# Kernel tuning notes

Hardware: AMD Instinct MI355X
Metric: run time of the kernel (lower is better)

## Reference

```python
import jax, jax.numpy as jnp
import numpy as np

B, S, N_EMBD = 4, 4096, 1024
HIDDEN = 4 * N_EMBD
M_BITS_FC = 3
M_BITS_PROJ = 3
BLOCK_K = 32


def block_quant(v, m_bits, bk):
    """Block-floating-point quantization along the last (K) dim.
    Each block of `bk` elements shares an exponent derived from its max-abs;
    mantissas are rounded to `m_bits` bits. Straight-through estimator for grads."""
    *lead, K = v.shape
    vb = v.reshape(*lead, K // bk, bk)
    amax = jnp.max(jnp.abs(vb), axis=-1, keepdims=True)
    tiny = jnp.asarray(2.0 ** -126, v.dtype)
    e = jnp.floor(jnp.log2(jnp.maximum(amax, tiny)))  # shared block exponent
    scale = jnp.exp2(e - m_bits)                       # quantization step
    q = jnp.round(vb / scale) * scale
    q = vb + jax.lax.stop_gradient(q - vb)             # STE
    return q.reshape(v.shape)


def lowprec_linear(x, w, b, m_bits, bk):
    # w: [out, in]; quantize both operands along the contraction dim.
    xq = block_quant(x, m_bits, bk)
    wq = block_quant(w, m_bits, bk)
    return jnp.einsum('bsk,nk->bsn', xq, wq) + b


def setup_inputs() -> dict:
    key = jax.random.key(0)
    k0, k1, k2 = jax.random.split(key, 3)
    x = jax.random.normal(k0, (B, S, N_EMBD), jnp.float32)
    w_fc = jax.random.normal(k1, (HIDDEN, N_EMBD), jnp.float32) * (1.0 / np.sqrt(N_EMBD))
    b_fc = jnp.zeros((HIDDEN,), jnp.float32)
    w_proj = jax.random.normal(k2, (N_EMBD, HIDDEN), jnp.float32) * (1.0 / np.sqrt(HIDDEN))
    b_proj = jnp.zeros((N_EMBD,), jnp.float32)
    return {"x": x, "w_fc": w_fc, "b_fc": b_fc, "w_proj": w_proj, "b_proj": b_proj}


def reference(x, w_fc, b_fc, w_proj, b_proj):
    h = lowprec_linear(x, w_fc, b_fc, M_BITS_FC, BLOCK_K)
    h = jax.nn.gelu(h, approximate=False)  # nn.GELU default = exact erf
    return lowprec_linear(h, w_proj, b_proj, M_BITS_PROJ, BLOCK_K)
```

## Files before the change

### kernel.cpp

```cpp
#include <hip/hip_runtime.h>
#include <hip/hip_bf16.h>

using bf16 = __hip_bfloat16;
typedef __attribute__((ext_vector_type(8))) short short8;
typedef __attribute__((ext_vector_type(4))) float f32x4;

#define DI __device__ __forceinline__

constexpr int MROWS = 16384;
constexpr int EMB   = 1024;
constexpr int HID   = 4096;

DI void gload16(const bf16* g, bf16* l) {
  __builtin_amdgcn_global_load_lds((const __attribute__((address_space(1))) void*)g,
                                   (__attribute__((address_space(3))) void*)l,
                                   16, 0, 0);
}

DI void qparams(float amax, float& scale, float& inv) {
  int eb = (int)((__float_as_uint(amax) >> 23) & 255u);
  eb = eb < 4 ? 4 : eb;
  scale = __uint_as_float((unsigned)(eb - 3) << 23);
  inv   = __uint_as_float((unsigned)(257 - eb) << 23);
}

__global__ void quant32(const float* __restrict__ in, bf16* __restrict__ out, int nblk) {
  int b = blockIdx.x * blockDim.x + threadIdx.x;
  if (b >= nblk) return;
  const float4* p = (const float4*)(in + (size_t)b * 32);
  float4 v[8];
  float amax = 0.f;
#pragma unroll
  for (int i = 0; i < 8; i++) {
    v[i] = p[i];
    amax = fmaxf(amax, fmaxf(fmaxf(fabsf(v[i].x), fabsf(v[i].y)),
                             fmaxf(fabsf(v[i].z), fabsf(v[i].w))));
  }
  float scale, inv;
  qparams(amax, scale, inv);
  alignas(16) unsigned short us[32];
#pragma unroll
  for (int i = 0; i < 8; i++) {
    us[i * 4 + 0] = (unsigned short)(__float_as_uint(rintf(v[i].x * inv) * scale) >> 16);
    us[i * 4 + 1] = (unsigned short)(__float_as_uint(rintf(v[i].y * inv) * scale) >> 16);
    us[i * 4 + 2] = (unsigned short)(__float_as_uint(rintf(v[i].z * inv) * scale) >> 16);
    us[i * 4 + 3] = (unsigned short)(__float_as_uint(rintf(v[i].w * inv) * scale) >> 16);
  }
  short8* o = (short8*)(out + (size_t)b * 32);
#pragma unroll
  for (int i = 0; i < 4; i++) o[i] = *(short8*)(us + i * 8);
}

#define MFMA16(a, b, c) __builtin_amdgcn_mfma_f32_16x16x32_bf16(a, b, c, 0, 0, 0)
#define SBAR()    __builtin_amdgcn_s_barrier()
#define WAITVM(n) asm volatile("s_waitcnt vmcnt(" #n ")" ::: "memory")

#define Q_MFMA(MB, NB, BG) \
  __builtin_amdgcn_s_setprio(1); \
  _Pragma("unroll") for (int kk = 0; kk < 2; kk++) \
  _Pragma("unroll") for (int mi = 0; mi < 4; mi++) \
  _Pragma("unroll") for (int ni = 0; ni < 2; ni++) \
    acc[(MB) + mi][(NB) + ni] = MFMA16(af[mi * 2 + kk], BG[ni * 2 + kk], acc[(MB) + mi][(NB) + ni]); \
  __builtin_amdgcn_s_setprio(0);

#define RD_A(mh) \
  _Pragma("unroll") for (int mi = 0; mi < 4; mi++) { \
    af[mi * 2]     = ldA(db, mh, mi, 0); \
    af[mi * 2 + 1] = ldA(db, mh, mi, 1); }

#define RD_B(half, dst) \
  _Pragma("unroll") for (int ni = 0; ni < 2; ni++) { \
    dst[ni * 2]     = ldB(db, half, ni, 0); \
    dst[ni * 2 + 1] = ldB(db, half, ni, 1); }

template<int Kd, int Nd, bool GQ>
__global__ void __launch_bounds__(512, 2)
gemm8(const bf16* __restrict__ Ap, const bf16* __restrict__ Bp,
      const float* __restrict__ bias, void* __restrict__ Cout) {
  __shared__ alignas(16) bf16 SH[65536];
  bf16* Abuf = SH;
  bf16* Bbuf = SH + 32768;

  const int tid  = threadIdx.x;
  const int lane = tid & 63, wave = tid >> 6;
  const int l16  = lane & 15, lhi = lane >> 4;
  const int wr   = wave >> 2, wc  = wave & 3;

  const int idx  = blockIdx.x >> 3;
  const int xid  = blockIdx.x & 7;
  const int brow = (xid * 8 + (idx & 7)) * 256;
  const int bcol = (idx >> 3) * 256;

  const int r0 = tid >> 3;
  const int sl = (tid & 7) ^ (r0 & 7);
  const bf16* asrc = Ap + (size_t)(brow + r0) * Kd + sl * 8;
  const bf16* bsrc = Bp + (size_t)(bcol + r0) * Kd + sl * 8;

  auto stA = [&](int tt, int half) {
    const bf16* s = asrc + (size_t)half * 128 * Kd + tt * 64;
    bf16* d = Abuf + ((tt & 1) * 2 + half) * 8192 + tid * 8;
    gload16(s, d); gload16(s + (size_t)64 * Kd, d + 4096);
  };
  auto stB = [&](int tt, int half) {
    const bf16* s = bsrc + (size_t)half * 128 * Kd + tt * 64;
    bf16* d = Bbuf + ((tt & 1) * 2 + half) * 8192 + tid * 8;
    gload16(s, d); gload16(s + (size_t)64 * Kd, d + 4096);
  };

  const int sx = l16 & 7;
  const int arow = wr * 16 + l16;
  auto ldA = [&](int db, int mh, int mi, int kk) -> short8 {
    return *(const short8*)(Abuf + (db * 2 + mh) * 8192 +
                            (mi * 32 + arow) * 64 + ((kk * 4 + lhi) ^ sx) * 8);
  };
  const int brl = wc * 32 + l16;
  auto ldB = [&](int db, int half, int ni, int kk) -> short8 {
    return *(const short8*)(Bbuf + (db * 2 + half) * 8192 +
                            (brl + ni * 16) * 64 + ((kk * 4 + lhi) ^ sx) * 8);
  };

  f32x4 acc[8][4] = {};
  short8 af[8], bgl[4], bgh[4];

  constexpr int NT = Kd / 64;

  stA(0, 0); stB(0, 0); stB(0, 1); stA(0, 1);
  stA(1, 0); stB(1, 0); stB(1, 1);
  WAITVM(6); SBAR();

  for (int t = 0; t <= NT - 3; ++t) {
    const int db = t & 1;
    stA(t + 1, 1);
    RD_A(0) RD_B(0, bgl)
    SBAR();
    Q_MFMA(0, 0, bgl)
    SBAR();
    stA(t + 2, 0);
    RD_B(1, bgh)
    SBAR();
    Q_MFMA(0, 2, bgh)
    SBAR();
    stB(t + 2, 0);
    RD_A(1)
    SBAR();
    Q_MFMA(4, 0, bgl)
    SBAR();
    stB(t + 2, 1);
    Q_MFMA(4, 2, bgh)
    WAITVM(6); SBAR();
  }

  {
    const int db = (NT - 2) & 1;
    stA(NT - 1, 1);
    RD_A(0) RD_B(0, bgl)
    SBAR();
    Q_MFMA(0, 0, bgl)
    SBAR();
    RD_B(1, bgh)
    SBAR();
    Q_MFMA(0, 2, bgh)
    SBAR();
    RD_A(1)
    SBAR();
    Q_MFMA(4, 0, bgl)
    SBAR();
    Q_MFMA(4, 2, bgh)
    WAITVM(0); SBAR();
  }

  {
    const int db = (NT - 1) & 1;
    RD_A(0) RD_B(0, bgl)
    Q_MFMA(0, 0, bgl)
    RD_B(1, bgh)
    Q_MFMA(0, 2, bgh)
    RD_A(1)
    Q_MFMA(4, 0, bgl)
    Q_MFMA(4, 2, bgh)
  }

  const int cb = bcol + wc * 32;
  float bv[4];
#pragma unroll
  for (int n = 0; n < 4; n++) bv[n] = bias[cb + (n >> 1) * 128 + (n & 1) * 16 + l16];

  if constexpr (GQ) {
    SBAR();
#pragma unroll
    for (int m = 0; m < 8; m++) {
      const int rl0 = m * 32 + wr * 16 + lhi * 4;
#pragma unroll
      for (int r = 0; r < 4; r++) {
        float g[4];
#pragma unroll
        for (int n = 0; n < 4; n++) {
          float v = acc[m][n][r] + bv[n];
          g[n] = 0.5f * v * (1.0f + erff(v * 0.70710678118654752f));
        }
#pragma unroll
        for (int p = 0; p < 2; p++) {
          float am = fmaxf(fabsf(g[p * 2]), fabsf(g[p * 2 + 1]));
#pragma unroll
          for (int msk = 1; msk <= 8; msk <<= 1) am = fmaxf(am, __shfl_xor(am, msk, 64));
          float sc, iv; qparams(am, sc, iv);
          const int co = (rl0 + r) * 256 + wc * 32 + p * 128 + l16;
          SH[co]      = __float2bfloat16(rintf(g[p * 2]     * iv) * sc);
          SH[co + 16] = __float2bfloat16(rintf(g[p * 2 + 1] * iv) * sc);
        }
      }
    }
    SBAR();
    bf16* outp = (bf16*)Cout;
#pragma unroll
    for (int i = 0; i < 16; i++) {
      const int c   = i * 512 + tid;
      const int row = c >> 5, cc = c & 31;
      *(short8*)(outp + (size_t)(brow + row) * Nd + bcol + cc * 8) =
          *(const short8*)(SH + (size_t)c * 8);
    }
  } else {
    float* outp = (float*)Cout;
#pragma unroll
    for (int m = 0; m < 8; m++) {
      const size_t rbase = (size_t)(brow + m * 32 + wr * 16 + lhi * 4);
#pragma unroll
      for (int r = 0; r < 4; r++) {
        const size_t ro = (rbase + r) * Nd;
#pragma unroll
        for (int n = 0; n < 4; n++)
          outp[ro + cb + (n >> 1) * 128 + (n & 1) * 16 + l16] = acc[m][n][r] + bv[n];
      }
    }
  }
}

extern "C" void kernel_launch(void* const* d_in, const int* in_sizes, int n_in,
                              void* d_out, int out_size, void* d_ws, size_t ws_size,
                              hipStream_t stream) {
  const float* x      = (const float*)d_in[0];
  const float* w_fc   = (const float*)d_in[1];
  const float* b_fc   = (const float*)d_in[2];
  const float* w_proj = (const float*)d_in[3];
  const float* b_proj = (const float*)d_in[4];

  char* ws = (char*)d_ws;
  bf16* xq  = (bf16*)ws;  ws += (size_t)MROWS * EMB * 2;
  bf16* wfq = (bf16*)ws;  ws += (size_t)HID * EMB * 2;
  bf16* wpq = (bf16*)ws;  ws += (size_t)EMB * HID * 2;
  bf16* hq  = (bf16*)ws;

  quant32<<<(MROWS * EMB / 32 + 255) / 256, 256, 0, stream>>>(x, xq, MROWS * EMB / 32);
  quant32<<<(HID * EMB / 32 + 255) / 256, 256, 0, stream>>>(w_fc, wfq, HID * EMB / 32);
  quant32<<<(EMB * HID / 32 + 255) / 256, 256, 0, stream>>>(w_proj, wpq, EMB * HID / 32);

  gemm8<EMB, HID, true ><<<(MROWS / 256) * (HID / 256), 512, 0, stream>>>(xq, wfq, b_fc, hq);
  gemm8<HID, EMB, false><<<(MROWS / 256) * (EMB / 256), 512, 0, stream>>>(hq, wpq, b_proj, (float*)d_out);
}
```

Before: 357.6 us.

## Remove intra-tile barriers, hoist LDS fragment reads, and swizzle GELU epilogue staging

Removes most s_barrier calls inside the K-loop, reading A and both B fragment halves at the start of each tile and interleaving the global-to-LDS stores with the MFMA groups. This cuts barrier stalls between waves. Separately, the GQ epilogue XOR-swizzles columns when staging quantized GELU output in LDS, and un-swizzles on the vector readback, to reduce bank conflicts. Dropping the barriers risks LDS races, since stores into the buffer not being read now happen without intermediate syncs, and holding more fragments in registers raises pressure.

```diff
diff --git a/kernel.cpp b/kernel.cpp
--- a/kernel.cpp
+++ b/kernel.cpp
@@ -63,7 +63,7 @@
     acc[(MB) + mi][(NB) + ni] = MFMA16(af[mi * 2 + kk], BG[ni * 2 + kk], acc[(MB) + mi][(NB) + ni]); \
   __builtin_amdgcn_s_setprio(0);
 
-#define RD_A(mh) \
+#define RD_AF(mh) \
   _Pragma("unroll") for (int mi = 0; mi < 4; mi++) { \
     af[mi * 2]     = ldA(db, mh, mi, 0); \
     af[mi * 2 + 1] = ldA(db, mh, mi, 1); }
@@ -130,52 +130,37 @@
 
   for (int t = 0; t <= NT - 3; ++t) {
     const int db = t & 1;
+    RD_AF(0) RD_B(0, bgl) RD_B(1, bgh)
     stA(t + 1, 1);
-    RD_A(0) RD_B(0, bgl)
-    SBAR();
     Q_MFMA(0, 0, bgl)
-    SBAR();
     stA(t + 2, 0);
-    RD_B(1, bgh)
-    SBAR();
     Q_MFMA(0, 2, bgh)
-    SBAR();
     stB(t + 2, 0);
-    RD_A(1)
-    SBAR();
+    RD_AF(1)
+    stB(t + 2, 1);
     Q_MFMA(4, 0, bgl)
-    SBAR();
-    stB(t + 2, 1);
     Q_MFMA(4, 2, bgh)
     WAITVM(6); SBAR();
   }
 
   {
     const int db = (NT - 2) & 1;
+    RD_AF(0) RD_B(0, bgl) RD_B(1, bgh)
     stA(NT - 1, 1);
-    RD_A(0) RD_B(0, bgl)
-    SBAR();
     Q_MFMA(0, 0, bgl)
-    SBAR();
-    RD_B(1, bgh)
-    SBAR();
     Q_MFMA(0, 2, bgh)
-    SBAR();
-    RD_A(1)
-    SBAR();
+    RD_AF(1)
     Q_MFMA(4, 0, bgl)
-    SBAR();
     Q_MFMA(4, 2, bgh)
     WAITVM(0); SBAR();
   }
 
   {
     const int db = (NT - 1) & 1;
-    RD_A(0) RD_B(0, bgl)
+    RD_AF(0) RD_B(0, bgl) RD_B(1, bgh)
     Q_MFMA(0, 0, bgl)
-    RD_B(1, bgh)
     Q_MFMA(0, 2, bgh)
-    RD_A(1)
+    RD_AF(1)
     Q_MFMA(4, 0, bgl)
     Q_MFMA(4, 2, bgh)
   }
@@ -204,9 +189,10 @@
 #pragma unroll
           for (int msk = 1; msk <= 8; msk <<= 1) am = fmaxf(am, __shfl_xor(am, msk, 64));
           float sc, iv; qparams(am, sc, iv);
-          const int co = (rl0 + r) * 256 + wc * 32 + p * 128 + l16;
-          SH[co]      = __float2bfloat16(rintf(g[p * 2]     * iv) * sc);
-          SH[co + 16] = __float2bfloat16(rintf(g[p * 2 + 1] * iv) * sc);
+          const int rowb = (rl0 + r) * 256;
+          const int c0   = wc * 32 + p * 128;
+          SH[rowb + ((c0 + l16)      ^ (lhi << 3))] = __float2bfloat16(rintf(g[p * 2]     * iv) * sc);
+          SH[rowb + ((c0 + 16 + l16) ^ (lhi << 3))] = __float2bfloat16(rintf(g[p * 2 + 1] * iv) * sc);
         }
       }
     }
@@ -216,8 +202,9 @@
     for (int i = 0; i < 16; i++) {
       const int c   = i * 512 + tid;
       const int row = c >> 5, cc = c & 31;
+      const int scc = cc ^ ((row >> 2) & 3);
       *(short8*)(outp + (size_t)(brow + row) * Nd + bcol + cc * 8) =
-          *(const short8*)(SH + (size_t)c * 8);
+          *(const short8*)(SH + (size_t)row * 256 + scc * 8);
     }
   } else {
     float* outp = (float*)Cout;
```

Result: faster. 344.9 us (-3.5%).
